# Performance work log

Measured on AMD Instinct MI355X. Metric: run time of the kernel, lower is better.

Reference implementation:

```python
import jax, jax.numpy as jnp
import numpy as np

N = 50000
E = 600000
H = 128      # hidden_dim
HEADS = 8
DH = H // HEADS  # 16, per-head dim
NEG_SLOPE = 0.2
LN_EPS = 1e-5


def setup_inputs() -> dict:
    key = jax.random.key(0)
    ks = jax.random.split(key, 20)
    rn = lambda k, shape, s=0.05: jax.random.normal(k, shape, jnp.float32) * s
    inp = {}
    inp["x"] = jax.random.normal(ks[0], (N, 2), jnp.float32)
    inp["edge_index"] = jax.random.randint(ks[1], (2, E), 0, N)
    inp["node_types"] = jax.random.randint(ks[2], (N,), 0, 3)
    inp["W_in"] = rn(ks[3], (2, H)); inp["b_in"] = jnp.zeros((H,), jnp.float32)
    for l in range(3):
        inp[f"gat_W{l}"] = rn(ks[4 + l], (H, H))          # lin weight (no bias in PyG GAT lin)
        inp[f"gat_as{l}"] = rn(ks[7 + l], (HEADS, DH))     # att_src
        inp[f"gat_ad{l}"] = rn(ks[10 + l], (HEADS, DH))    # att_dst
        inp[f"gat_b{l}"] = jnp.zeros((H,), jnp.float32)    # output bias (concat heads)
        inp[f"ln_g{l}"] = jnp.ones((H,), jnp.float32)
        inp[f"ln_b{l}"] = jnp.zeros((H,), jnp.float32)
    inp["W1"] = rn(ks[13], (H, H)); inp["b1"] = jnp.zeros((H,), jnp.float32)
    inp["W2"] = rn(ks[14], (H, H // 2)); inp["b2"] = jnp.zeros((H // 2,), jnp.float32)
    inp["W3"] = rn(ks[15], (H // 2, 1)); inp["b3"] = jnp.zeros((1,), jnp.float32)
    return inp


def layer_norm(x, g, b):
    mu = jnp.mean(x, axis=-1, keepdims=True)
    var = jnp.mean(jnp.square(x - mu), axis=-1, keepdims=True)
    return (x - mu) * jax.lax.rsqrt(var + LN_EPS) * g + b


def gat_conv(x, src, dst, W, a_src, a_dst, bias):
    # PyG GATConv, eval mode (no dropout), concat=True.
    h = (x @ W).reshape(N, HEADS, DH)                     # [N,He,Dh]
    alpha_s = jnp.einsum("nhd,hd->nh", h, a_src)           # [N,He]
    alpha_d = jnp.einsum("nhd,hd->nh", h, a_dst)
    e = jax.nn.leaky_relu(alpha_s[src] + alpha_d[dst], NEG_SLOPE)  # [E,He]
    # segment softmax over incoming edges of each dst node
    e = e - jax.ops.segment_max(e, dst, num_segments=N)[dst]
    ex = jnp.exp(e)
    denom = jax.ops.segment_sum(ex, dst, num_segments=N)[dst]
    alpha = ex / denom                                     # [E,He]
    msg = h[src] * alpha[..., None]                        # [E,He,Dh]
    out = jax.ops.segment_sum(msg, dst, num_segments=N)    # [N,He,Dh]
    return out.reshape(N, H) + bias


def reference(x, edge_index, node_types,
              W_in, b_in,
              gat_W0, gat_as0, gat_ad0, gat_b0, ln_g0, ln_b0,
              gat_W1, gat_as1, gat_ad1, gat_b1, ln_g1, ln_b1,
              gat_W2, gat_as2, gat_ad2, gat_b2, ln_g2, ln_b2,
              W1, b1, W2, b2, W3, b3):
    # add self loops (PyG GATConv default add_self_loops=True)
    loops = jnp.arange(N, dtype=edge_index.dtype)
    src = jnp.concatenate([edge_index[0], loops])
    dst = jnp.concatenate([edge_index[1], loops])

    h = x @ W_in + b_in
    layers = [(gat_W0, gat_as0, gat_ad0, gat_b0, ln_g0, ln_b0),
              (gat_W1, gat_as1, gat_ad1, gat_b1, ln_g1, ln_b1),
              (gat_W2, gat_as2, gat_ad2, gat_b2, ln_g2, ln_b2)]
    for (W, a_s, a_d, b, g, beta) in layers:
        res = h
        h = jax.nn.relu(gat_conv(h, src, dst, W, a_s, a_d, b))
        h = layer_norm(h + res, g, beta)
    # batch is None -> no pooling; MLP head per node
    h = jax.nn.relu(h @ W1 + b1)
    h = jax.nn.relu(h @ W2 + b2)
    return h @ W3 + b3   # [N,1]
```

## Files before the change

kernel.cpp:

```cpp
#include <hip/hip_runtime.h>
#include <hip/hip_bf16.h>
#include <hip/hip_fp16.h>

#define NN 50000
#define EE 600000
#define CAP 64

typedef __attribute__((ext_vector_type(8))) short bfrag;
typedef __attribute__((ext_vector_type(4))) float f4;
#define MFMA16 __builtin_amdgcn_mfma_f32_16x16x32_bf16

__device__ __forceinline__ float bf2f(unsigned short u) {
    return __uint_as_float(((unsigned int)u) << 16);
}
__device__ __forceinline__ unsigned short f2bf(float f) {
    unsigned int u = __float_as_uint(f);
    unsigned int r = (u + 0x7fffu + ((u >> 16) & 1u)) >> 16;
    return (unsigned short)r;
}
__device__ __forceinline__ float lrelu(float x) { return x > 0.f ? x : 0.2f * x; }

__global__ void k_detect(const unsigned short* __restrict__ win,
                         int* __restrict__ dflag) {
    __shared__ float red[256];
    int t = threadIdx.x;
    red[t] = fabsf(bf2f(win[t]));
    __syncthreads();
    for (int s = 128; s > 0; s >>= 1) {
        if (t < s) red[t] = fmaxf(red[t], red[t + s]);
        __syncthreads();
    }
    if (t == 0) {
        float mb = red[0];
        *dflag = (mb > 1.0f) ? 2 : ((mb < 1e-3f) ? 1 : 0);
    }
}

struct ConvDesc { const void* src; float* dst; int n; int blk_start; };
struct ConvTable { ConvDesc d[27]; int nd; };

__global__ void k_convert_all(ConvTable T, const int* __restrict__ dflag) {
    int b = blockIdx.x;
    int ti = 0;
    for (int i = 0; i < T.nd; ++i) if (b >= T.d[i].blk_start) ti = i;
    int local = (b - T.d[ti].blk_start) * 256 + threadIdx.x;
    int n = T.d[ti].n;
    if (local >= n) return;
    int f = *dflag;
    float v;
    if (f == 2) {
        v = ((const float*)T.d[ti].src)[local];
    } else {
        unsigned short u = ((const unsigned short*)T.d[ti].src)[local];
        if (f == 0) v = bf2f(u);
        else { __half h = *(const __half*)&u; v = __half2float(h); }
    }
    T.d[ti].dst[local] = v;
}

struct WsDesc { const float* W; const float* avS; const float* avD;
                unsigned short* hi; unsigned short* lo;
                int T; int ldw; int elem_start; };
struct WsTable { WsDesc d[5]; int nd; int total; };

__global__ void k_wswizzle(WsTable TB) {
    int e = blockIdx.x * 256 + threadIdx.x;
    if (e >= TB.total) return;
    int ti = 0;
    for (int i = 0; i < TB.nd; ++i) if (e >= TB.d[i].elem_start) ti = i;
    WsDesc D = TB.d[ti];
    int le = e - D.elem_start;
    int c = le / (D.T * 64);
    int rem = le % (D.T * 64);
    int tt = rem / 64, L = rem % 64;
    int q = L >> 4, n = L & 15;
    bool synth = (D.avS != nullptr) && (tt == D.T - 1);
    for (int j = 0; j < 8; ++j) {
        int k = c * 32 + q * 8 + j;
        float v;
        if (synth) {
            int hd = (n < 8) ? n : (n - 8);
            const float* av = (n < 8) ? D.avS : D.avD;
            v = 0.f;
            for (int d2 = 0; d2 < 16; ++d2)
                v += D.W[k * D.ldw + hd * 16 + d2] * av[hd * 16 + d2];
        } else {
            v = D.W[k * D.ldw + tt * 16 + n];
        }
        unsigned short h = f2bf(v);
        D.hi[(size_t)le * 8 + j] = h;
        D.lo[(size_t)le * 8 + j] = f2bf(v - bf2f(h));
    }
}

__global__ void k_zero(int* __restrict__ p, int n) {
    int i = blockIdx.x * 256 + threadIdx.x;
    if (i < n) p[i] = 0;
}

__global__ void k_fill_csr(const int* __restrict__ src, const int* __restrict__ dst,
                           int* __restrict__ cursor, int* __restrict__ col) {
    int i = blockIdx.x * 256 + threadIdx.x;
    if (i < EE) {
        int d = dst[i];
        int p = atomicAdd(&cursor[d], 1);
        if (p < CAP) col[d * CAP + p] = src[i];
    }
}

__global__ void k_input_proj(const float* __restrict__ xf,
                             const float* __restrict__ Winf,
                             const float* __restrict__ binf,
                             unsigned short* __restrict__ hhi,
                             unsigned short* __restrict__ hlo) {
    int i = blockIdx.x * 256 + threadIdx.x;
    if (i >= NN * 128) return;
    int n = i >> 7, j = i & 127;
    float v = xf[2 * n] * Winf[j] + xf[2 * n + 1] * Winf[128 + j] + binf[j];
    unsigned short h = f2bf(v);
    hhi[i] = h;
    hlo[i] = f2bf(v - bf2f(h));
}

__global__ __launch_bounds__(256) void k_gat_lin_mfma(
    const unsigned short* __restrict__ hhi, const unsigned short* __restrict__ hlo,
    const unsigned short* __restrict__ Bhi, const unsigned short* __restrict__ Blo,
    unsigned short* __restrict__ hb, float* __restrict__ alS, float* __restrict__ alD) {
    const int t = threadIdx.x, w = t >> 6, lane = t & 63;
    const int row0 = blockIdx.x * 64 + w * 16;
    int arow = row0 + (lane & 15); if (arow > NN - 1) arow = NN - 1;
    const int q = lane >> 4, colL = lane & 15;
    const unsigned short* ah = hhi + (size_t)arow * 128 + q * 8;
    const unsigned short* al = hlo + (size_t)arow * 128 + q * 8;
    f4 acc[9] = {};
#pragma unroll
    for (int c = 0; c < 4; ++c) {
        bfrag ahif = *(const bfrag*)(ah + c * 32);
        bfrag alof = *(const bfrag*)(al + c * 32);
        const unsigned short* bp  = Bhi + ((size_t)(c * 9) * 64 + lane) * 8;
        const unsigned short* bpl = Blo + ((size_t)(c * 9) * 64 + lane) * 8;
#pragma unroll
        for (int tt = 0; tt < 9; ++tt) {
            bfrag bh = *(const bfrag*)(bp  + (size_t)tt * 512);
            bfrag bl = *(const bfrag*)(bpl + (size_t)tt * 512);
            acc[tt] = MFMA16(ahif, bh, acc[tt], 0, 0, 0);
            acc[tt] = MFMA16(alof, bh, acc[tt], 0, 0, 0);
            acc[tt] = MFMA16(ahif, bl, acc[tt], 0, 0, 0);
        }
    }
#pragma unroll
    for (int r = 0; r < 4; ++r) {
        int row = row0 + q * 4 + r;
        if (row < NN) {
#pragma unroll
            for (int tt = 0; tt < 8; ++tt)
                hb[(size_t)row * 128 + tt * 16 + colL] = f2bf(acc[tt][r]);
            if (colL < 8) alS[row * 8 + colL] = acc[8][r];
            else          alD[row * 8 + colL - 8] = acc[8][r];
        }
    }
}

__global__ void k_gat_agg(const unsigned short* __restrict__ hb,
                          const float* __restrict__ alS, const float* __restrict__ alD,
                          const int* __restrict__ deg, const int* __restrict__ col,
                          const float* __restrict__ bias, const float* __restrict__ lng,
                          const float* __restrict__ lnb,
                          unsigned short* __restrict__ hhi,
                          unsigned short* __restrict__ hlo) {
    int n = (blockIdx.x * 256 + threadIdx.x) >> 6;
    int lane = threadIdx.x & 63;
    if (n >= NN) return;
    int c0 = lane << 1;
    int head = lane >> 3;
    float ad = alD[n * 8 + head];
    float sw = __expf(lrelu(alS[n * 8 + head] + ad));
    ushort2 hv = *(const ushort2*)(hb + (size_t)n * 128 + c0);
    float den = sw, a0 = sw * bf2f(hv.x), a1 = sw * bf2f(hv.y);
    int d = deg[n]; if (d > CAP) d = CAP; if (d < 0) d = 0;
    const int* cl = col + n * CAP;
    int j = 0;
    for (; j + 4 <= d; j += 4) {
        int4 ss = *(const int4*)(cl + j);
        float e0 = alS[(size_t)ss.x * 8 + head];
        float e1 = alS[(size_t)ss.y * 8 + head];
        float e2 = alS[(size_t)ss.z * 8 + head];
        float e3 = alS[(size_t)ss.w * 8 + head];
        ushort2 r0 = *(const ushort2*)(hb + (size_t)ss.x * 128 + c0);
        ushort2 r1 = *(const ushort2*)(hb + (size_t)ss.y * 128 + c0);
        ushort2 r2 = *(const ushort2*)(hb + (size_t)ss.z * 128 + c0);
        ushort2 r3 = *(const ushort2*)(hb + (size_t)ss.w * 128 + c0);
        float w0 = __expf(lrelu(e0 + ad));
        float w1 = __expf(lrelu(e1 + ad));
        float w2 = __expf(lrelu(e2 + ad));
        float w3 = __expf(lrelu(e3 + ad));
        den += (w0 + w1) + (w2 + w3);
        a0 = fmaf(w0, bf2f(r0.x), a0); a1 = fmaf(w0, bf2f(r0.y), a1);
        a0 = fmaf(w1, bf2f(r1.x), a0); a1 = fmaf(w1, bf2f(r1.y), a1);
        a0 = fmaf(w2, bf2f(r2.x), a0); a1 = fmaf(w2, bf2f(r2.y), a1);
        a0 = fmaf(w3, bf2f(r3.x), a0); a1 = fmaf(w3, bf2f(r3.y), a1);
    }
    for (; j < d; ++j) {
        int s = cl[j];
        float wj = __expf(lrelu(alS[(size_t)s * 8 + head] + ad));
        ushort2 hj = *(const ushort2*)(hb + (size_t)s * 128 + c0);
        den += wj;
        a0 = fmaf(wj, bf2f(hj.x), a0);
        a1 = fmaf(wj, bf2f(hj.y), a1);
    }
    float inv = 1.f / den;
    ushort2 rh = *(const ushort2*)(hhi + (size_t)n * 128 + c0);
    ushort2 rl = *(const ushort2*)(hlo + (size_t)n * 128 + c0);
    float v0 = fmaxf(fmaf(a0, inv, bias[c0]), 0.f) + (bf2f(rh.x) + bf2f(rl.x));
    float v1 = fmaxf(fmaf(a1, inv, bias[c0 + 1]), 0.f) + (bf2f(rh.y) + bf2f(rl.y));
    float s = v0 + v1;
#pragma unroll
    for (int m = 1; m < 64; m <<= 1) s += __shfl_xor(s, m, 64);
    float mean = s * (1.f / 128.f);
    float d0 = v0 - mean, d1 = v1 - mean;
    float q = d0 * d0 + d1 * d1;
#pragma unroll
    for (int m = 1; m < 64; m <<= 1) q += __shfl_xor(q, m, 64);
    float invstd = rsqrtf(q * (1.f / 128.f) + 1e-5f);
    float o0 = d0 * invstd * lng[c0] + lnb[c0];
    float o1 = d1 * invstd * lng[c0 + 1] + lnb[c0 + 1];
    unsigned short h0 = f2bf(o0), h1 = f2bf(o1);
    *(ushort2*)(hhi + (size_t)n * 128 + c0) = make_ushort2(h0, h1);
    *(ushort2*)(hlo + (size_t)n * 128 + c0) =
        make_ushort2(f2bf(o0 - bf2f(h0)), f2bf(o1 - bf2f(h1)));
}

__global__ __launch_bounds__(256) void k_mlp_mfma(
    const unsigned short* __restrict__ hhi, const unsigned short* __restrict__ hlo,
    const unsigned short* __restrict__ W1hi, const unsigned short* __restrict__ W1lo,
    const float* __restrict__ b1,
    const unsigned short* __restrict__ W2hi, const unsigned short* __restrict__ W2lo,
    const float* __restrict__ b2,
    const float* __restrict__ W3, const float* __restrict__ b3,
    void* __restrict__ out, const int* __restrict__ dflag) {
    __shared__ unsigned short z1hi[64 * 136];
    __shared__ unsigned short z1lo[64 * 136];
    __shared__ float z2s[64 * 68];
    const int t = threadIdx.x, w = t >> 6, lane = t & 63;
    const int row0 = blockIdx.x * 64 + w * 16;
    const int q = lane >> 4, colL = lane & 15;
    int arow = row0 + colL; if (arow > NN - 1) arow = NN - 1;
    const int lrow = w * 16 + q * 4;
    {
        const unsigned short* ah = hhi + (size_t)arow * 128 + q * 8;
        const unsigned short* al = hlo + (size_t)arow * 128 + q * 8;
        f4 acc[8] = {};
#pragma unroll
        for (int c = 0; c < 4; ++c) {
            bfrag ahif = *(const bfrag*)(ah + c * 32);
            bfrag alof = *(const bfrag*)(al + c * 32);
            const unsigned short* bp  = W1hi + ((size_t)(c * 8) * 64 + lane) * 8;
            const unsigned short* bpl = W1lo + ((size_t)(c * 8) * 64 + lane) * 8;
#pragma unroll
            for (int tt = 0; tt < 8; ++tt) {
                bfrag bh = *(const bfrag*)(bp  + (size_t)tt * 512);
                bfrag bl = *(const bfrag*)(bpl + (size_t)tt * 512);
                acc[tt] = MFMA16(ahif, bh, acc[tt], 0, 0, 0);
                acc[tt] = MFMA16(alof, bh, acc[tt], 0, 0, 0);
                acc[tt] = MFMA16(ahif, bl, acc[tt], 0, 0, 0);
            }
        }
#pragma unroll
        for (int r = 0; r < 4; ++r)
#pragma unroll
            for (int tt = 0; tt < 8; ++tt) {
                float v = fmaxf(acc[tt][r] + b1[tt * 16 + colL], 0.f);
                unsigned short h = f2bf(v);
                z1hi[(lrow + r) * 136 + tt * 16 + colL] = h;
                z1lo[(lrow + r) * 136 + tt * 16 + colL] = f2bf(v - bf2f(h));
            }
    }
    __syncthreads();
    {
        const int zrow = w * 16 + colL;
        f4 acc[4] = {};
#pragma unroll
        for (int c = 0; c < 4; ++c) {
            bfrag ahif = *(const bfrag*)(z1hi + zrow * 136 + c * 32 + q * 8);
            bfrag alof = *(const bfrag*)(z1lo + zrow * 136 + c * 32 + q * 8);
            const unsigned short* bp  = W2hi + ((size_t)(c * 4) * 64 + lane) * 8;
            const unsigned short* bpl = W2lo + ((size_t)(c * 4) * 64 + lane) * 8;
#pragma unroll
            for (int tt = 0; tt < 4; ++tt) {
                bfrag bh = *(const bfrag*)(bp  + (size_t)tt * 512);
                bfrag bl = *(const bfrag*)(bpl + (size_t)tt * 512);
                acc[tt] = MFMA16(ahif, bh, acc[tt], 0, 0, 0);
                acc[tt] = MFMA16(alof, bh, acc[tt], 0, 0, 0);
                acc[tt] = MFMA16(ahif, bl, acc[tt], 0, 0, 0);
            }
        }
#pragma unroll
        for (int r = 0; r < 4; ++r)
#pragma unroll
            for (int tt = 0; tt < 4; ++tt)
                z2s[(lrow + r) * 68 + tt * 16 + colL] =
                    fmaxf(acc[tt][r] + b2[tt * 16 + colL], 0.f);
    }
    __syncthreads();
    {
        int row = t >> 2, quarter = t & 3;
        const float* zp = z2s + row * 68 + quarter * 16;
        float v = 0.f;
#pragma unroll
        for (int i = 0; i < 16; ++i) v += zp[i] * W3[quarter * 16 + i];
        v += __shfl_xor(v, 1, 64);
        v += __shfl_xor(v, 2, 64);
        if (quarter == 0) {
            int gr = blockIdx.x * 64 + row;
            if (gr < NN) {
                float r = v + b3[0];
                int f = *dflag;
                if (f == 2) ((float*)out)[gr] = r;
                else if (f == 1) { __half hh = __float2half(r); ((unsigned short*)out)[gr] = *(unsigned short*)&hh; }
                else ((unsigned short*)out)[gr] = f2bf(r);
            }
        }
    }
}

extern "C" void kernel_launch(void* const* d_in, const int* in_sizes, int n_in,
                              void* d_out, int out_size, void* d_ws, size_t ws_size,
                              hipStream_t stream) {
    if (n_in != 29) { hipMemsetAsync(d_out, 0x41, (size_t)out_size * 2, stream); return; }
    if (in_sizes[0] != 100000 || in_sizes[1] != 1200000 ||
        in_sizes[3] != 256 || in_sizes[5] != 16384) {
        hipMemsetAsync(d_out, 0x43, (size_t)out_size * 2, stream); return;
    }
    if (ws_size < 60ull * 1024 * 1024) {
        hipMemsetAsync(d_out, 0x42, (size_t)out_size * 2, stream); return;
    }

    char* ws = (char*)d_ws;
    auto alloc = [&](size_t nbytes) -> char* {
        char* p = ws; ws += (nbytes + 255) & ~(size_t)255; return p;
    };
    float* xf   = (float*)alloc(100000 * 4);
    float* Winf = (float*)alloc(256 * 4);
    float* binf = (float*)alloc(128 * 4);
    float *Wf[3], *asf[3], *adf[3], *gbf[3], *lgf[3], *lbf[3];
    for (int l = 0; l < 3; ++l) {
        Wf[l]  = (float*)alloc(16384 * 4);
        asf[l] = (float*)alloc(128 * 4);
        adf[l] = (float*)alloc(128 * 4);
        gbf[l] = (float*)alloc(128 * 4);
        lgf[l] = (float*)alloc(128 * 4);
        lbf[l] = (float*)alloc(128 * 4);
    }
    float* W1f = (float*)alloc(16384 * 4);
    float* b1f = (float*)alloc(128 * 4);
    float* W2f = (float*)alloc(8192 * 4);
    float* b2f = (float*)alloc(64 * 4);
    float* W3f = (float*)alloc(64 * 4);
    float* b3f = (float*)alloc(4);
    unsigned short *Gsw_hi[3], *Gsw_lo[3];
    for (int l = 0; l < 3; ++l) {
        Gsw_hi[l] = (unsigned short*)alloc(2304 * 8 * 2);
        Gsw_lo[l] = (unsigned short*)alloc(2304 * 8 * 2);
    }
    unsigned short* W1sw_hi = (unsigned short*)alloc(2048 * 8 * 2);
    unsigned short* W1sw_lo = (unsigned short*)alloc(2048 * 8 * 2);
    unsigned short* W2sw_hi = (unsigned short*)alloc(1024 * 8 * 2);
    unsigned short* W2sw_lo = (unsigned short*)alloc(1024 * 8 * 2);
    unsigned short* hhi = (unsigned short*)alloc((size_t)NN * 128 * 2);
    unsigned short* hlo = (unsigned short*)alloc((size_t)NN * 128 * 2);
    unsigned short* hb  = (unsigned short*)alloc((size_t)NN * 128 * 2);
    float* alS  = (float*)alloc((size_t)NN * 8 * 4);
    float* alD  = (float*)alloc((size_t)NN * 8 * 4);
    int* cursor = (int*)alloc((size_t)NN * 4);
    int* col    = (int*)alloc((size_t)NN * CAP * 4);
    int* dflag  = (int*)alloc(4);

    k_detect<<<1, 256, 0, stream>>>((const unsigned short*)d_in[3], dflag);

    ConvTable T; int nb = 0, e = 0;
    auto add = [&](const void* src, float* dst, int n) {
        T.d[e].src = src; T.d[e].dst = dst; T.d[e].n = n;
        T.d[e].blk_start = nb; nb += (n + 255) / 256; ++e;
    };
    add(d_in[0], xf, 100000);
    add(d_in[3], Winf, 256);
    add(d_in[4], binf, 128);
    for (int l = 0; l < 3; ++l) {
        add(d_in[5 + 6 * l], Wf[l], 16384);
        add(d_in[6 + 6 * l], asf[l], 128);
        add(d_in[7 + 6 * l], adf[l], 128);
        add(d_in[8 + 6 * l], gbf[l], 128);
        add(d_in[9 + 6 * l], lgf[l], 128);
        add(d_in[10 + 6 * l], lbf[l], 128);
    }
    add(d_in[23], W1f, 16384);
    add(d_in[24], b1f, 128);
    add(d_in[25], W2f, 8192);
    add(d_in[26], b2f, 64);
    add(d_in[27], W3f, 64);
    add(d_in[28], b3f, 1);
    T.nd = e;
    k_convert_all<<<nb, 256, 0, stream>>>(T, dflag);

    WsTable WT; int es = 0; int wd = 0;
    auto addw = [&](const float* W, const float* avS, const float* avD,
                    unsigned short* hi, unsigned short* lo, int Tt, int ldw) {
        WT.d[wd].W = W; WT.d[wd].avS = avS; WT.d[wd].avD = avD;
        WT.d[wd].hi = hi; WT.d[wd].lo = lo; WT.d[wd].T = Tt; WT.d[wd].ldw = ldw;
        WT.d[wd].elem_start = es; es += 4 * Tt * 64; ++wd;
    };
    for (int l = 0; l < 3; ++l)
        addw(Wf[l], asf[l], adf[l], Gsw_hi[l], Gsw_lo[l], 9, 128);
    addw(W1f, nullptr, nullptr, W1sw_hi, W1sw_lo, 8, 128);
    addw(W2f, nullptr, nullptr, W2sw_hi, W2sw_lo, 4, 64);
    WT.nd = wd; WT.total = es;
    k_wswizzle<<<(es + 255) / 256, 256, 0, stream>>>(WT);

    const int* ei = (const int*)d_in[1];
    k_zero<<<(NN + 255) / 256, 256, 0, stream>>>(cursor, NN);
    k_fill_csr<<<(EE + 255) / 256, 256, 0, stream>>>(ei, ei + EE, cursor, col);
    k_input_proj<<<(NN * 128) / 256, 256, 0, stream>>>(xf, Winf, binf, hhi, hlo);

    const int gemm_blocks = (NN + 63) / 64;
    for (int l = 0; l < 3; ++l) {
        k_gat_lin_mfma<<<gemm_blocks, 256, 0, stream>>>(
            hhi, hlo, Gsw_hi[l], Gsw_lo[l], hb, alS, alD);
        k_gat_agg<<<NN / 4, 256, 0, stream>>>(hb, alS, alD, cursor, col,
                                              gbf[l], lgf[l], lbf[l], hhi, hlo);
    }
    k_mlp_mfma<<<gemm_blocks, 256, 0, stream>>>(
        hhi, hlo, W1sw_hi, W1sw_lo, b1f, W2sw_hi, W2sw_lo, b2f,
        W3f, b3f, d_out, dflag);
}
```

Before: 369.8 us.

## Precompute per-edge attention weights in LDS and fold cursor zeroing into convert

The aggregation kernel now computes each edge's exp(leaky_relu) attention weight once per (edge, head) with all 64 lanes cooperating, and stores the weights in shared memory. Previously each weight was recomputed by all 8 lanes of a head, and the scattered alS loads were duplicated the same way. The separate cursor-zeroing kernel is removed by adding a null-source entry to the conversion table that writes zeros. The cost is a block-wide barrier and 8 KB of LDS per wave, and the early-exit bound check is gone, which is safe only because NN divides by 4.

```diff
diff --git a/kernel.cpp b/kernel.cpp
--- a/kernel.cpp
+++ b/kernel.cpp
@@ -37,7 +37,7 @@
 }
 
 struct ConvDesc { const void* src; float* dst; int n; int blk_start; };
-struct ConvTable { ConvDesc d[27]; int nd; };
+struct ConvTable { ConvDesc d[28]; int nd; };
 
 __global__ void k_convert_all(ConvTable T, const int* __restrict__ dflag) {
     int b = blockIdx.x;
@@ -46,6 +46,7 @@
     int local = (b - T.d[ti].blk_start) * 256 + threadIdx.x;
     int n = T.d[ti].n;
     if (local >= n) return;
+    if (T.d[ti].src == nullptr) { T.d[ti].dst[local] = 0.f; return; }
     int f = *dflag;
     float v;
     if (f == 2) {
@@ -93,11 +94,6 @@
     }
 }
 
-__global__ void k_zero(int* __restrict__ p, int n) {
-    int i = blockIdx.x * 256 + threadIdx.x;
-    if (i < n) p[i] = 0;
-}
-
 __global__ void k_fill_csr(const int* __restrict__ src, const int* __restrict__ dst,
                            int* __restrict__ cursor, int* __restrict__ col) {
     int i = blockIdx.x * 256 + threadIdx.x;
@@ -161,39 +157,50 @@
     }
 }
 
-__global__ void k_gat_agg(const unsigned short* __restrict__ hb,
-                          const float* __restrict__ alS, const float* __restrict__ alD,
-                          const int* __restrict__ deg, const int* __restrict__ col,
-                          const float* __restrict__ bias, const float* __restrict__ lng,
-                          const float* __restrict__ lnb,
-                          unsigned short* __restrict__ hhi,
-                          unsigned short* __restrict__ hlo) {
-    int n = (blockIdx.x * 256 + threadIdx.x) >> 6;
-    int lane = threadIdx.x & 63;
-    if (n >= NN) return;
-    int c0 = lane << 1;
-    int head = lane >> 3;
+__global__ __launch_bounds__(256) void k_gat_agg(
+    const unsigned short* __restrict__ hb,
+    const float* __restrict__ alS, const float* __restrict__ alD,
+    const int* __restrict__ deg, const int* __restrict__ col,
+    const float* __restrict__ bias, const float* __restrict__ lng,
+    const float* __restrict__ lnb,
+    unsigned short* __restrict__ hhi, unsigned short* __restrict__ hlo) {
+    __shared__ float wlds[4][CAP * 8];
+    const int wv = threadIdx.x >> 6;
+    const int n = blockIdx.x * 4 + wv;
+    const int lane = threadIdx.x & 63;
+    int d = deg[n]; if (d > CAP) d = CAP; if (d < 0) d = 0;
+    const int* cl = col + n * CAP;
+    {
+        const int headp = lane & 7, jl = lane >> 3;
+        const float adp = alD[n * 8 + headp];
+        for (int j0 = 0; j0 < d; j0 += 8) {
+            int j = j0 + jl;
+            if (j < d) {
+                int s = cl[j];
+                wlds[wv][j * 8 + headp] =
+                    __expf(lrelu(alS[(size_t)s * 8 + headp] + adp));
+            }
+        }
+    }
+    __syncthreads();
+    const int c0 = lane << 1;
+    const int head = lane >> 3;
     float ad = alD[n * 8 + head];
     float sw = __expf(lrelu(alS[n * 8 + head] + ad));
     ushort2 hv = *(const ushort2*)(hb + (size_t)n * 128 + c0);
     float den = sw, a0 = sw * bf2f(hv.x), a1 = sw * bf2f(hv.y);
-    int d = deg[n]; if (d > CAP) d = CAP; if (d < 0) d = 0;
-    const int* cl = col + n * CAP;
+    const float* wp = wlds[wv];
     int j = 0;
     for (; j + 4 <= d; j += 4) {
         int4 ss = *(const int4*)(cl + j);
-        float e0 = alS[(size_t)ss.x * 8 + head];
-        float e1 = alS[(size_t)ss.y * 8 + head];
-        float e2 = alS[(size_t)ss.z * 8 + head];
-        float e3 = alS[(size_t)ss.w * 8 + head];
+        float w0 = wp[(j + 0) * 8 + head];
+        float w1 = wp[(j + 1) * 8 + head];
+        float w2 = wp[(j + 2) * 8 + head];
+        float w3 = wp[(j + 3) * 8 + head];
         ushort2 r0 = *(const ushort2*)(hb + (size_t)ss.x * 128 + c0);
         ushort2 r1 = *(const ushort2*)(hb + (size_t)ss.y * 128 + c0);
         ushort2 r2 = *(const ushort2*)(hb + (size_t)ss.z * 128 + c0);
         ushort2 r3 = *(const ushort2*)(hb + (size_t)ss.w * 128 + c0);
-        float w0 = __expf(lrelu(e0 + ad));
-        float w1 = __expf(lrelu(e1 + ad));
-        float w2 = __expf(lrelu(e2 + ad));
-        float w3 = __expf(lrelu(e3 + ad));
         den += (w0 + w1) + (w2 + w3);
         a0 = fmaf(w0, bf2f(r0.x), a0); a1 = fmaf(w0, bf2f(r0.y), a1);
         a0 = fmaf(w1, bf2f(r1.x), a0); a1 = fmaf(w1, bf2f(r1.y), a1);
@@ -202,7 +209,7 @@
     }
     for (; j < d; ++j) {
         int s = cl[j];
-        float wj = __expf(lrelu(alS[(size_t)s * 8 + head] + ad));
+        float wj = wp[j * 8 + head];
         ushort2 hj = *(const ushort2*)(hb + (size_t)s * 128 + c0);
         den += wj;
         a0 = fmaf(wj, bf2f(hj.x), a0);
@@ -399,6 +406,7 @@
     add(d_in[26], b2f, 64);
     add(d_in[27], W3f, 64);
     add(d_in[28], b3f, 1);
+    add(nullptr, (float*)cursor, NN);
     T.nd = e;
     k_convert_all<<<nb, 256, 0, stream>>>(T, dflag);
 
@@ -417,7 +425,6 @@
     k_wswizzle<<<(es + 255) / 256, 256, 0, stream>>>(WT);
 
     const int* ei = (const int*)d_in[1];
-    k_zero<<<(NN + 255) / 256, 256, 0, stream>>>(cursor, NN);
     k_fill_csr<<<(EE + 255) / 256, 256, 0, stream>>>(ei, ei + EE, cursor, col);
     k_input_proj<<<(NN * 128) / 256, 256, 0, stream>>>(xf, Winf, binf, hhi, hlo);
 
```

Measured after the change: 396.3 us. 7.2% more time.

## Fold input projection into layer-0 GAT linear via precomposed rank-2 weights

Applied to the files above, without the earlier changes.

Precomputes W_in@W0, b_in@W0 and their attention projections in a tiny kernel. Layer 0's transformed features and attention logits then come from the 2-dim input directly, which skips the first MFMA GEMM. Cursor zeroing is merged into the conversion kernel to drop a launch, and the aggregation gather loop is unrolled to 8 edges. Slight numeric differences from reassociation and extra register pressure in the aggregation kernel are possible.

```diff
diff --git a/kernel.cpp b/kernel.cpp
--- a/kernel.cpp
+++ b/kernel.cpp
@@ -37,7 +37,7 @@
 }
 
 struct ConvDesc { const void* src; float* dst; int n; int blk_start; };
-struct ConvTable { ConvDesc d[27]; int nd; };
+struct ConvTable { ConvDesc d[28]; int nd; };
 
 __global__ void k_convert_all(ConvTable T, const int* __restrict__ dflag) {
     int b = blockIdx.x;
@@ -46,6 +46,7 @@
     int local = (b - T.d[ti].blk_start) * 256 + threadIdx.x;
     int n = T.d[ti].n;
     if (local >= n) return;
+    if (T.d[ti].src == nullptr) { T.d[ti].dst[local] = 0.f; return; }
     int f = *dflag;
     float v;
     if (f == 2) {
@@ -61,7 +62,7 @@
 struct WsDesc { const float* W; const float* avS; const float* avD;
                 unsigned short* hi; unsigned short* lo;
                 int T; int ldw; int elem_start; };
-struct WsTable { WsDesc d[5]; int nd; int total; };
+struct WsTable { WsDesc d[4]; int nd; int total; };
 
 __global__ void k_wswizzle(WsTable TB) {
     int e = blockIdx.x * 256 + threadIdx.x;
@@ -93,9 +94,45 @@
     }
 }
 
-__global__ void k_zero(int* __restrict__ p, int n) {
-    int i = blockIdx.x * 256 + threadIdx.x;
-    if (i < n) p[i] = 0;
+__global__ void k_prep0(const float* __restrict__ Winf, const float* __restrict__ binf,
+                        const float* __restrict__ W0,
+                        const float* __restrict__ as0, const float* __restrict__ ad0,
+                        float* __restrict__ Wc, float* __restrict__ bc,
+                        float* __restrict__ ASc, float* __restrict__ ADc) {
+    __shared__ float WcS[256];
+    __shared__ float bcS[128];
+    int t = threadIdx.x;
+    int r = t >> 7, c = t & 127;
+    float acc = 0.f;
+    for (int k = 0; k < 128; ++k) acc += Winf[r * 128 + k] * W0[k * 128 + c];
+    WcS[t] = acc;
+    Wc[t] = acc;
+    if (r == 0) {
+        float ab = 0.f;
+        for (int k = 0; k < 128; ++k) ab += binf[k] * W0[k * 128 + c];
+        bcS[c] = ab;
+        bc[c] = ab;
+    }
+    __syncthreads();
+    if (t < 8) {
+#pragma unroll
+        for (int rr = 0; rr < 2; ++rr) {
+            float a = 0.f, b = 0.f;
+            for (int d2 = 0; d2 < 16; ++d2) {
+                a += WcS[rr * 128 + t * 16 + d2] * as0[t * 16 + d2];
+                b += WcS[rr * 128 + t * 16 + d2] * ad0[t * 16 + d2];
+            }
+            ASc[rr * 8 + t] = a;
+            ADc[rr * 8 + t] = b;
+        }
+        float a = 0.f, b = 0.f;
+        for (int d2 = 0; d2 < 16; ++d2) {
+            a += bcS[t * 16 + d2] * as0[t * 16 + d2];
+            b += bcS[t * 16 + d2] * ad0[t * 16 + d2];
+        }
+        ASc[16 + t] = a;
+        ADc[16 + t] = b;
+    }
 }
 
 __global__ void k_fill_csr(const int* __restrict__ src, const int* __restrict__ dst,
@@ -108,18 +145,29 @@
     }
 }
 
-__global__ void k_input_proj(const float* __restrict__ xf,
-                             const float* __restrict__ Winf,
-                             const float* __restrict__ binf,
-                             unsigned short* __restrict__ hhi,
-                             unsigned short* __restrict__ hlo) {
+__global__ void k_layer0(const float* __restrict__ xf,
+                         const float* __restrict__ Winf, const float* __restrict__ binf,
+                         const float* __restrict__ Wc, const float* __restrict__ bc,
+                         const float* __restrict__ ASc, const float* __restrict__ ADc,
+                         unsigned short* __restrict__ hhi, unsigned short* __restrict__ hlo,
+                         unsigned short* __restrict__ hb,
+                         float* __restrict__ alS, float* __restrict__ alD) {
     int i = blockIdx.x * 256 + threadIdx.x;
     if (i >= NN * 128) return;
     int n = i >> 7, j = i & 127;
-    float v = xf[2 * n] * Winf[j] + xf[2 * n + 1] * Winf[128 + j] + binf[j];
-    unsigned short h = f2bf(v);
+    float x0 = xf[2 * n], x1 = xf[2 * n + 1];
+    float h0 = fmaf(x0, Winf[j], fmaf(x1, Winf[128 + j], binf[j]));
+    unsigned short h = f2bf(h0);
     hhi[i] = h;
-    hlo[i] = f2bf(v - bf2f(h));
+    hlo[i] = f2bf(h0 - bf2f(h));
+    float v = fmaf(x0, Wc[j], fmaf(x1, Wc[128 + j], bc[j]));
+    hb[i] = f2bf(v);
+    if (j < 8)
+        alS[n * 8 + j] = fmaf(x0, ASc[j], fmaf(x1, ASc[8 + j], ASc[16 + j]));
+    else if (j < 16) {
+        int hh = j - 8;
+        alD[n * 8 + hh] = fmaf(x0, ADc[hh], fmaf(x1, ADc[8 + hh], ADc[16 + hh]));
+    }
 }
 
 __global__ __launch_bounds__(256) void k_gat_lin_mfma(
@@ -161,16 +209,15 @@
     }
 }
 
-__global__ void k_gat_agg(const unsigned short* __restrict__ hb,
-                          const float* __restrict__ alS, const float* __restrict__ alD,
-                          const int* __restrict__ deg, const int* __restrict__ col,
-                          const float* __restrict__ bias, const float* __restrict__ lng,
-                          const float* __restrict__ lnb,
-                          unsigned short* __restrict__ hhi,
-                          unsigned short* __restrict__ hlo) {
+__global__ __launch_bounds__(256) void k_gat_agg(
+    const unsigned short* __restrict__ hb,
+    const float* __restrict__ alS, const float* __restrict__ alD,
+    const int* __restrict__ deg, const int* __restrict__ col,
+    const float* __restrict__ bias, const float* __restrict__ lng,
+    const float* __restrict__ lnb,
+    unsigned short* __restrict__ hhi, unsigned short* __restrict__ hlo) {
     int n = (blockIdx.x * 256 + threadIdx.x) >> 6;
     int lane = threadIdx.x & 63;
-    if (n >= NN) return;
     int c0 = lane << 1;
     int head = lane >> 3;
     float ad = alD[n * 8 + head];
@@ -180,25 +227,44 @@
     int d = deg[n]; if (d > CAP) d = CAP; if (d < 0) d = 0;
     const int* cl = col + n * CAP;
     int j = 0;
-    for (; j + 4 <= d; j += 4) {
-        int4 ss = *(const int4*)(cl + j);
-        float e0 = alS[(size_t)ss.x * 8 + head];
-        float e1 = alS[(size_t)ss.y * 8 + head];
-        float e2 = alS[(size_t)ss.z * 8 + head];
-        float e3 = alS[(size_t)ss.w * 8 + head];
-        ushort2 r0 = *(const ushort2*)(hb + (size_t)ss.x * 128 + c0);
-        ushort2 r1 = *(const ushort2*)(hb + (size_t)ss.y * 128 + c0);
-        ushort2 r2 = *(const ushort2*)(hb + (size_t)ss.z * 128 + c0);
-        ushort2 r3 = *(const ushort2*)(hb + (size_t)ss.w * 128 + c0);
+    for (; j + 8 <= d; j += 8) {
+        int4 sa = *(const int4*)(cl + j);
+        int4 sb = *(const int4*)(cl + j + 4);
+        int s0 = sa.x, s1 = sa.y, s2 = sa.z, s3 = sa.w;
+        int s4 = sb.x, s5 = sb.y, s6 = sb.z, s7 = sb.w;
+        float e0 = alS[(size_t)s0 * 8 + head];
+        float e1 = alS[(size_t)s1 * 8 + head];
+        float e2 = alS[(size_t)s2 * 8 + head];
+        float e3 = alS[(size_t)s3 * 8 + head];
+        float e4 = alS[(size_t)s4 * 8 + head];
+        float e5 = alS[(size_t)s5 * 8 + head];
+        float e6 = alS[(size_t)s6 * 8 + head];
+        float e7 = alS[(size_t)s7 * 8 + head];
+        ushort2 r0 = *(const ushort2*)(hb + (size_t)s0 * 128 + c0);
+        ushort2 r1 = *(const ushort2*)(hb + (size_t)s1 * 128 + c0);
+        ushort2 r2 = *(const ushort2*)(hb + (size_t)s2 * 128 + c0);
+        ushort2 r3 = *(const ushort2*)(hb + (size_t)s3 * 128 + c0);
+        ushort2 r4 = *(const ushort2*)(hb + (size_t)s4 * 128 + c0);
+        ushort2 r5 = *(const ushort2*)(hb + (size_t)s5 * 128 + c0);
+        ushort2 r6 = *(const ushort2*)(hb + (size_t)s6 * 128 + c0);
+        ushort2 r7 = *(const ushort2*)(hb + (size_t)s7 * 128 + c0);
         float w0 = __expf(lrelu(e0 + ad));
         float w1 = __expf(lrelu(e1 + ad));
         float w2 = __expf(lrelu(e2 + ad));
         float w3 = __expf(lrelu(e3 + ad));
-        den += (w0 + w1) + (w2 + w3);
+        float w4 = __expf(lrelu(e4 + ad));
+        float w5 = __expf(lrelu(e5 + ad));
+        float w6 = __expf(lrelu(e6 + ad));
+        float w7 = __expf(lrelu(e7 + ad));
+        den += ((w0 + w1) + (w2 + w3)) + ((w4 + w5) + (w6 + w7));
         a0 = fmaf(w0, bf2f(r0.x), a0); a1 = fmaf(w0, bf2f(r0.y), a1);
         a0 = fmaf(w1, bf2f(r1.x), a0); a1 = fmaf(w1, bf2f(r1.y), a1);
         a0 = fmaf(w2, bf2f(r2.x), a0); a1 = fmaf(w2, bf2f(r2.y), a1);
         a0 = fmaf(w3, bf2f(r3.x), a0); a1 = fmaf(w3, bf2f(r3.y), a1);
+        a0 = fmaf(w4, bf2f(r4.x), a0); a1 = fmaf(w4, bf2f(r4.y), a1);
+        a0 = fmaf(w5, bf2f(r5.x), a0); a1 = fmaf(w5, bf2f(r5.y), a1);
+        a0 = fmaf(w6, bf2f(r6.x), a0); a1 = fmaf(w6, bf2f(r6.y), a1);
+        a0 = fmaf(w7, bf2f(r7.x), a0); a1 = fmaf(w7, bf2f(r7.y), a1);
     }
     for (; j < d; ++j) {
         int s = cl[j];
@@ -357,8 +423,8 @@
     float* b2f = (float*)alloc(64 * 4);
     float* W3f = (float*)alloc(64 * 4);
     float* b3f = (float*)alloc(4);
-    unsigned short *Gsw_hi[3], *Gsw_lo[3];
-    for (int l = 0; l < 3; ++l) {
+    unsigned short *Gsw_hi[2], *Gsw_lo[2];
+    for (int l = 0; l < 2; ++l) {
         Gsw_hi[l] = (unsigned short*)alloc(2304 * 8 * 2);
         Gsw_lo[l] = (unsigned short*)alloc(2304 * 8 * 2);
     }
@@ -366,6 +432,10 @@
     unsigned short* W1sw_lo = (unsigned short*)alloc(2048 * 8 * 2);
     unsigned short* W2sw_hi = (unsigned short*)alloc(1024 * 8 * 2);
     unsigned short* W2sw_lo = (unsigned short*)alloc(1024 * 8 * 2);
+    float* Wc  = (float*)alloc(256 * 4);
+    float* bc  = (float*)alloc(128 * 4);
+    float* ASc = (float*)alloc(24 * 4);
+    float* ADc = (float*)alloc(24 * 4);
     unsigned short* hhi = (unsigned short*)alloc((size_t)NN * 128 * 2);
     unsigned short* hlo = (unsigned short*)alloc((size_t)NN * 128 * 2);
     unsigned short* hb  = (unsigned short*)alloc((size_t)NN * 128 * 2);
@@ -399,6 +469,7 @@
     add(d_in[26], b2f, 64);
     add(d_in[27], W3f, 64);
     add(d_in[28], b3f, 1);
+    add(nullptr, (float*)cursor, NN);
     T.nd = e;
     k_convert_all<<<nb, 256, 0, stream>>>(T, dflag);
 
@@ -409,22 +480,26 @@
         WT.d[wd].hi = hi; WT.d[wd].lo = lo; WT.d[wd].T = Tt; WT.d[wd].ldw = ldw;
         WT.d[wd].elem_start = es; es += 4 * Tt * 64; ++wd;
     };
-    for (int l = 0; l < 3; ++l)
-        addw(Wf[l], asf[l], adf[l], Gsw_hi[l], Gsw_lo[l], 9, 128);
+    addw(Wf[1], asf[1], adf[1], Gsw_hi[0], Gsw_lo[0], 9, 128);
+    addw(Wf[2], asf[2], adf[2], Gsw_hi[1], Gsw_lo[1], 9, 128);
     addw(W1f, nullptr, nullptr, W1sw_hi, W1sw_lo, 8, 128);
     addw(W2f, nullptr, nullptr, W2sw_hi, W2sw_lo, 4, 64);
     WT.nd = wd; WT.total = es;
     k_wswizzle<<<(es + 255) / 256, 256, 0, stream>>>(WT);
+    k_prep0<<<1, 256, 0, stream>>>(Winf, binf, Wf[0], asf[0], adf[0],
+                                   Wc, bc, ASc, ADc);
 
     const int* ei = (const int*)d_in[1];
-    k_zero<<<(NN + 255) / 256, 256, 0, stream>>>(cursor, NN);
     k_fill_csr<<<(EE + 255) / 256, 256, 0, stream>>>(ei, ei + EE, cursor, col);
-    k_input_proj<<<(NN * 128) / 256, 256, 0, stream>>>(xf, Winf, binf, hhi, hlo);
+    k_layer0<<<(NN * 128) / 256, 256, 0, stream>>>(
+        xf, Winf, binf, Wc, bc, ASc, ADc, hhi, hlo, hb, alS, alD);
 
     const int gemm_blocks = (NN + 63) / 64;
-    for (int l = 0; l < 3; ++l) {
+    k_gat_agg<<<NN / 4, 256, 0, stream>>>(hb, alS, alD, cursor, col,
+                                          gbf[0], lgf[0], lbf[0], hhi, hlo);
+    for (int l = 1; l < 3; ++l) {
         k_gat_lin_mfma<<<gemm_blocks, 256, 0, stream>>>(
-            hhi, hlo, Gsw_hi[l], Gsw_lo[l], hb, alS, alD);
+            hhi, hlo, Gsw_hi[l - 1], Gsw_lo[l - 1], hb, alS, alD);
         k_gat_agg<<<NN / 4, 256, 0, stream>>>(hb, alS, alD, cursor, col,
                                               gbf[l], lgf[l], lbf[l], hhi, hlo);
     }
```

After: 383.8 us. 3.8% more time.
